# Performance work log

Measured on AMD Instinct MI355X. Metric: run time of the kernel, lower is better.

## Reference

```python
import jax, jax.numpy as jnp
import numpy as np

K = 3        # prediction_steps
SKIP = 1     # skip_step (forward default)
NEG = 64     # opt.negative_samples
EPS = 1e-11  # ExpNLLLoss epsilon


def setup_inputs() -> dict:
    key = jax.random.key(0)
    ks = jax.random.split(key, 8)
    B, C, H, W = 64, 256, 14, 14
    z = jax.random.normal(ks[0], (B, C, H, W), jnp.float32)
    c = jax.random.normal(ks[1], (B, C, H, W), jnp.float32)
    Wk = jax.random.normal(ks[2], (K, C, C), jnp.float32) / np.sqrt(C).astype(np.float32)
    inp = {"z": z, "c": c, "Wk": Wk}
    for k in range(1, K + 1):
        Hp = H - (k + SKIP)
        rows = Hp * W * B
        inp[f"neg_idx_k{k}"] = jax.random.randint(ks[2 + k], (rows * NEG,), 0, rows, dtype=jnp.int32)
    return inp


def _loss_k(z, c, Wk, neg_idx, k):
    # z, c: [B,C,H,W]; Wk: [Co,Ci] (1x1 conv); neg_idx: [(H-k-SKIP)*W*B*NEG]
    B, C, H, W = z.shape
    Hp = H - (k + SKIP)
    zt = z[:, :, k + SKIP:, :]                            # [B,Ci,Hp,W]
    ztwk = jnp.einsum('oc,bchw->hwbo', Wk, zt)            # [Hp,W,B,Co] (1x1 conv + permute(2,3,0,1))
    flat = ztwk.reshape(Hp * W * B, -1)
    shuf = flat[neg_idx].reshape(Hp, W, B, NEG, -1)       # gathered negatives [Hp,W,B,N,Co]
    ctx = jnp.transpose(c[:, :, :Hp, :], (2, 3, 0, 1))    # context c[:,:,:-(k+SKIP),:] -> [Hp,W,B,Co]
    main = jnp.einsum('hwbc,hwbc->hwb', ctx, ztwk)[..., None]   # [Hp,W,B,1]
    negs = jnp.einsum('hwbc,hwbnc->hwbn', ctx, shuf)            # [Hp,W,B,N]
    log_fk = jnp.concatenate([main, negs], axis=-1)             # [Hp,W,B,1+N]
    log_fk = jnp.transpose(log_fk, (2, 3, 0, 1))                # [B,1+N,Hp,W]
    probs = jax.nn.softmax(log_fk, axis=1)
    # ExpNLLLoss, target class 0, reduction='mean'
    return -jnp.mean(jnp.log(probs[:, 0] + EPS))


def reference(z, c, Wk, neg_idx_k1, neg_idx_k2, neg_idx_k3):
    idxs = [neg_idx_k1, neg_idx_k2, neg_idx_k3]
    total = 0.0
    for k in range(1, K + 1):
        total = total + _loss_k(z, c, Wk[k - 1], idxs[k - 1], k)
    return total / K
```

## Files before the change

kernel.cpp:

```cpp
#include <hip/hip_runtime.h>
#include <math.h>


typedef short bf16x8 __attribute__((ext_vector_type(8)));
typedef float f32x4 __attribute__((ext_vector_type(4)));

static __device__ __forceinline__ unsigned short f2bf(float f) {
    union { float f; unsigned int u; } x; x.f = f;
    unsigned int r = x.u + 0x7fffu + ((x.u >> 16) & 1u);
    return (unsigned short)(r >> 16);
}

static __device__ __forceinline__ unsigned char f2e4m3(float f) {
    union { float f; unsigned int u; } x; x.f = f;
    unsigned int s = (x.u >> 24) & 0x80u;
    float af = fabsf(f);
    if (af > 448.f) af = 448.f;
    x.f = af;
    unsigned int u = x.u;
    int e = (int)(u >> 23) - 127;
    unsigned int out;
    if (af == 0.f) {
        out = 0u;
    } else if (e < -6) {
        int mq = (int)rintf(af * 512.f);
        out = (mq >= 8) ? 0x08u : (unsigned int)mq;
    } else {
        unsigned int r = u + 0x7FFFFu + ((u >> 20) & 1u);
        int e2 = (int)(r >> 23) - 127;
        if (e2 > 8) out = 0x7Eu;
        else out = (unsigned int)(((e2 + 7) << 3) | ((r >> 20) & 7u));
    }
    return (unsigned char)(s | out);
}

static __device__ __forceinline__ void gload_lds4(const void* g, void* l) {
    __builtin_amdgcn_global_load_lds(
        (const __attribute__((address_space(1))) void*)g,
        (__attribute__((address_space(3))) void*)l, 4, 0, 0);
}

__global__ __launch_bounds__(256)
void prep_kernel(const float* __restrict__ z, const float* __restrict__ c,
                 const float* __restrict__ Wk,
                 unsigned short* __restrict__ zt, unsigned char* __restrict__ ct8,
                 unsigned short* __restrict__ wkb, float* __restrict__ out) {
    __shared__ float tile[16][201];
    const int tid = threadIdx.x;
    int x = blockIdx.x;
    if (x < 768) {
        int i = x * 256 + tid;
        wkb[i] = f2bf(Wk[i]);
        if (x == 0 && tid == 0) out[0] = 0.f;
        return;
    }
    const bool isz = x < 1792;
    const int local = isz ? (x - 768) : (x - 1792);
    const float* src = isz ? z : c;
    const int b  = local & 63;
    const int c0 = (local >> 6) << 4;
    for (int i = tid; i < 16 * 196; i += 256) {
        int cc = i / 196;
        int hw = i - cc * 196;
        tile[cc][hw] = src[(size_t)((b << 8) + c0 + cc) * 196 + hw];
    }
    __syncthreads();
    if (isz) {
        for (int i = tid; i < 196 * 16; i += 256) {
            int hw = i >> 4, cc = i & 15;
            zt[(size_t)((hw << 6) + b) * 256 + c0 + cc] = f2bf(tile[cc][hw]);
        }
    } else {
        for (int i = tid; i < 196 * 16; i += 256) {
            int hw = i >> 4, cc = i & 15;
            ct8[(size_t)((hw << 6) + b) * 256 + c0 + cc] = f2e4m3(tile[cc][hw]);
        }
    }
}

#define PSTR 528
__global__ __launch_bounds__(256)
void proj_mfma_kernel(const unsigned short* __restrict__ zt,
                      const unsigned short* __restrict__ wkb,
                      unsigned char* __restrict__ ztwk) {
    __shared__ __align__(16) unsigned char smem[(64 + 32) * PSTR];
    unsigned char* smA = smem;
    unsigned char* smB = smem + 64 * PSTR;

    int x = blockIdx.y;
    int k, hw;
    if (x < 168)      { k = 0; hw = x; }
    else if (x < 322) { k = 1; hw = x - 168; }
    else              { k = 2; hw = x - 322; }
    const int o0 = blockIdx.x << 5;
    const int row0  = hw << 6;
    const int zrow0 = row0 + (((k + 2) * 14) << 6);
    unsigned char* zo = ztwk + (size_t)k * 10752 * 256;

    const int tid = threadIdx.x;
    const unsigned char* zsrc = (const unsigned char*)(zt + (size_t)zrow0 * 256);
    const unsigned char* bsrc = (const unsigned char*)(wkb + ((size_t)k << 16) + o0 * 256);

    #pragma unroll
    for (int i = 0; i < 8; ++i) {
        int sb = ((i << 8) + tid) << 4;
        int r = sb >> 9, off = sb & 511;
        *(int4*)(smA + r * PSTR + off) = *(const int4*)(zsrc + sb);
    }
    #pragma unroll
    for (int i = 0; i < 4; ++i) {
        int sb = ((i << 8) + tid) << 4;
        int r = sb >> 9, off = sb & 511;
        *(int4*)(smB + r * PSTR + off) = *(const int4*)(bsrc + sb);
    }
    __syncthreads();

    const int wv = tid >> 6, lane = tid & 63;
    const int m = lane & 15, kq = lane >> 4;
    f32x4 acc[2] = {};
    const unsigned short* aP  = (const unsigned short*)(smA + (size_t)((wv << 4) + m) * PSTR) + (kq << 3);
    const unsigned short* bP0 = (const unsigned short*)(smB + (size_t)m * PSTR) + (kq << 3);
    const unsigned short* bP1 = (const unsigned short*)(smB + (size_t)(16 + m) * PSTR) + (kq << 3);
    #pragma unroll
    for (int kk = 0; kk < 256; kk += 32) {
        bf16x8 af = *(const bf16x8*)(aP  + kk);
        bf16x8 b0 = *(const bf16x8*)(bP0 + kk);
        bf16x8 b1 = *(const bf16x8*)(bP1 + kk);
        acc[0] = __builtin_amdgcn_mfma_f32_16x16x32_bf16(af, b0, acc[0], 0, 0, 0);
        acc[1] = __builtin_amdgcn_mfma_f32_16x16x32_bf16(af, b1, acc[1], 0, 0, 0);
    }
    __syncthreads();
    unsigned char* cs = smA;
    #pragma unroll
    for (int nt = 0; nt < 2; ++nt)
        #pragma unroll
        for (int r = 0; r < 4; ++r)
            cs[(size_t)((wv << 4) + (kq << 2) + r) * 40 + (nt << 4) + m] =
                f2e4m3(acc[nt][r]);
    __syncthreads();
    {
        int r = tid >> 2, off = (tid & 3) << 3;
        unsigned long long v = *(const unsigned long long*)(cs + (size_t)r * 40 + off);
        *(unsigned long long*)(zo + (size_t)(row0 + r) * 256 + o0 + off) = v;
    }
}

#define ROWB 272
__global__ __launch_bounds__(128, 4)
void loss_mfma_kernel(const unsigned char* __restrict__ ct8,
                      const unsigned char* __restrict__ ztwk8,
                      const int* __restrict__ n0, const int* __restrict__ n1,
                      const int* __restrict__ n2, float* __restrict__ rowloss) {
    __shared__ __align__(16) unsigned char slab[65 * ROWB];
    __shared__ __align__(16) unsigned char ctx_s[256];
    __shared__ float sred[2][2];
    const int tid = threadIdx.x;
    const int wv = tid >> 6, lane = tid & 63;
    const int m = lane & 15, kq = lane >> 4;

    int x = blockIdx.x;
    int k; const int* nb_base;
    if (x < 10752)      { k = 0; nb_base = n0; }
    else if (x < 20608) { k = 1; nb_base = n1; x -= 10752; }
    else                { k = 2; nb_base = n2; x -= 20608; }
    const int row = x;
    const unsigned char* flat8 = ztwk8 + (size_t)k * 10752 * 256;
    const float wk = (k == 0) ? (1.f / (3.f * 10752.f))
                   : (k == 1) ? (1.f / (3.f * 9856.f))
                              : (1.f / (3.f * 8960.f));
    const int rbase = (k == 0) ? 0 : (k == 1) ? 10752 : 20608;

    const int myidx = nb_base[((size_t)row << 6) + lane];

    if (wv == 0) {
        gload_lds4(flat8 + (size_t)row * 256 + (lane << 2), slab);
        #pragma unroll
        for (int j = 1; j <= 32; ++j) {
            int idx = __builtin_amdgcn_readlane(myidx, j - 1);
            gload_lds4(flat8 + (size_t)idx * 256 + (lane << 2), slab + j * ROWB);
        }
    } else {
        gload_lds4(ct8 + (size_t)row * 256 + (lane << 2), ctx_s);
        #pragma unroll
        for (int j = 33; j <= 64; ++j) {
            int idx = __builtin_amdgcn_readlane(myidx, j - 1);
            gload_lds4(flat8 + (size_t)idx * 256 + (lane << 2), slab + j * ROWB);
        }
    }
    __syncthreads();

    f32x4 acc[3] = {};
    const int mt0 = (wv == 0) ? 0 : 3;
    int soff[3];
    #pragma unroll
    for (int t = 0; t < 3; ++t) {
        int slot = ((mt0 + t) << 4) + m;
        if (slot > 64) slot = 64;
        soff[t] = slot * ROWB + (kq << 3);
    }
    const unsigned char* cp = ctx_s + (kq << 3);
    #pragma unroll
    for (int kk = 0; kk < 8; ++kk) {
        long long bfrag = *(const long long*)(cp + (kk << 5));
        #pragma unroll
        for (int t = 0; t < 3; ++t) {
            if (t < 2 || wv == 0) {
                long long af = *(const long long*)(slab + soff[t] + (kk << 5));
                acc[t] = __builtin_amdgcn_mfma_f32_16x16x32_fp8_fp8(af, bfrag, acc[t], 0, 0, 0);
            }
        }
    }

    float m_l = -1e30f;
    if (wv == 0) {
        #pragma unroll
        for (int t = 0; t < 3; ++t)
            #pragma unroll
            for (int r = 0; r < 4; ++r) m_l = fmaxf(m_l, acc[t][r]);
    } else {
        #pragma unroll
        for (int r = 0; r < 4; ++r) m_l = fmaxf(m_l, acc[0][r]);
        if (kq == 0) m_l = fmaxf(m_l, acc[1][0]);
    }
    m_l = fmaxf(m_l, __shfl_xor(m_l, 16));
    m_l = fmaxf(m_l, __shfl_xor(m_l, 32));

    float s_l = 0.f;
    if (wv == 0) {
        #pragma unroll
        for (int t = 0; t < 3; ++t)
            #pragma unroll
            for (int r = 0; r < 4; ++r) s_l += __expf(acc[t][r] - m_l);
    } else {
        #pragma unroll
        for (int r = 0; r < 4; ++r) s_l += __expf(acc[0][r] - m_l);
        if (kq == 0) s_l += __expf(acc[1][0] - m_l);
    }
    s_l += __shfl_xor(s_l, 16);
    s_l += __shfl_xor(s_l, 32);

    float main_l = acc[0][0];
    if (lane == 0) { sred[wv][0] = m_l; sred[wv][1] = s_l; }
    __syncthreads();
    if (tid == 0) {
        float m0 = sred[0][0], s0 = sred[0][1];
        float m1 = sred[1][0], s1 = sred[1][1];
        float mg = fmaxf(m0, m1);
        float sg = s0 * __expf(m0 - mg) + s1 * __expf(m1 - mg);
        float p0 = __expf(main_l - mg) / sg;
        rowloss[rbase + row] = -logf(p0 + 1e-11f) * wk;
    }
}

__global__ __launch_bounds__(256)
void reduce_kernel(const float* __restrict__ rl, float* __restrict__ out) {
    float s = 0.f;
    const int stride = gridDim.x * blockDim.x;
    for (int i = blockIdx.x * blockDim.x + threadIdx.x; i < 29568; i += stride)
        s += rl[i];
    #pragma unroll
    for (int off = 32; off >= 1; off >>= 1) s += __shfl_xor(s, off);
    if ((threadIdx.x & 63) == 0) atomicAdd(out, s);
}

extern "C" void kernel_launch(void* const* d_in, const int* in_sizes, int n_in,
                              void* d_out, int out_size, void* d_ws, size_t ws_size,
                              hipStream_t stream) {
    const float* z  = (const float*)d_in[0];
    const float* c  = (const float*)d_in[1];
    const float* Wk = (const float*)d_in[2];
    const int* negs[3] = {(const int*)d_in[3], (const int*)d_in[4], (const int*)d_in[5]};
    float* out = (float*)d_out;

    char* p = (char*)d_ws;
    unsigned short* zt      = (unsigned short*)p;   p += (size_t)196 * 64 * 256 * 2;
    unsigned short* wkb     = (unsigned short*)p;   p += (size_t)3 * 65536 * 2;
    unsigned char*  ct8     = (unsigned char*)p;    p += (size_t)196 * 64 * 256;
    unsigned char*  ztwk8   = (unsigned char*)p;    p += (size_t)3 * 10752 * 256;
    float*          rowloss = (float*)p;

    prep_kernel<<<2816, 256, 0, stream>>>(z, c, Wk, zt, ct8, wkb, out);
    proj_mfma_kernel<<<dim3(8, 462), 256, 0, stream>>>(zt, wkb, ztwk8);
    loss_mfma_kernel<<<29568, 128, 0, stream>>>(ct8, ztwk8, negs[0], negs[1],
                                                negs[2], rowloss);
    reduce_kernel<<<32, 256, 0, stream>>>(rowloss, out);
}
```

Measured before the change: 157.9 us.

## Make loss kernel persistent with double-buffered gather prefetch

The loss kernel changes from one block per row to 1024 persistent blocks that stride over all rows. While the current row is computed, each block gathers the next row's negatives and context into a second LDS buffer, and it preloads the index list two rows ahead. Each block keeps its partial loss in a register and writes one value, so the reduce kernel shrinks to four blocks. This is meant to remove block launch and tail overhead and to hide gather latency, at the cost of twice the LDS per block and fewer resident waves per CU to cover memory latency.

After: 171.0 us. +8.3%, slower.

```diff
diff --git a/kernel.cpp b/kernel.cpp
--- a/kernel.cpp
+++ b/kernel.cpp
@@ -146,118 +146,178 @@
 }
 
 #define ROWB 272
-__global__ __launch_bounds__(128, 4)
+#define NBLK 1024
+
+static __device__ __forceinline__ void rowmeta(int gr, int* k, int* row) {
+    if (gr < 10752)      { *k = 0; *row = gr; }
+    else if (gr < 20608) { *k = 1; *row = gr - 10752; }
+    else                 { *k = 2; *row = gr - 20608; }
+}
+
+__global__ __launch_bounds__(128, 2)
 void loss_mfma_kernel(const unsigned char* __restrict__ ct8,
                       const unsigned char* __restrict__ ztwk8,
                       const int* __restrict__ n0, const int* __restrict__ n1,
                       const int* __restrict__ n2, float* __restrict__ rowloss) {
-    __shared__ __align__(16) unsigned char slab[65 * ROWB];
-    __shared__ __align__(16) unsigned char ctx_s[256];
-    __shared__ float sred[2][2];
+    __shared__ __align__(16) unsigned char slab[2][65 * ROWB];
+    __shared__ __align__(16) unsigned char ctxs[2][256];
+    __shared__ int idxb[2][64];
+    __shared__ float sred[2][2][4];
+
     const int tid = threadIdx.x;
     const int wv = tid >> 6, lane = tid & 63;
     const int m = lane & 15, kq = lane >> 4;
-
-    int x = blockIdx.x;
-    int k; const int* nb_base;
-    if (x < 10752)      { k = 0; nb_base = n0; }
-    else if (x < 20608) { k = 1; nb_base = n1; x -= 10752; }
-    else                { k = 2; nb_base = n2; x -= 20608; }
-    const int row = x;
-    const unsigned char* flat8 = ztwk8 + (size_t)k * 10752 * 256;
-    const float wk = (k == 0) ? (1.f / (3.f * 10752.f))
-                   : (k == 1) ? (1.f / (3.f * 9856.f))
-                              : (1.f / (3.f * 8960.f));
-    const int rbase = (k == 0) ? 0 : (k == 1) ? 10752 : 20608;
-
-    const int myidx = nb_base[((size_t)row << 6) + lane];
-
-    if (wv == 0) {
-        gload_lds4(flat8 + (size_t)row * 256 + (lane << 2), slab);
-        #pragma unroll
-        for (int j = 1; j <= 32; ++j) {
-            int idx = __builtin_amdgcn_readlane(myidx, j - 1);
-            gload_lds4(flat8 + (size_t)idx * 256 + (lane << 2), slab + j * ROWB);
-        }
-    } else {
-        gload_lds4(ct8 + (size_t)row * 256 + (lane << 2), ctx_s);
-        #pragma unroll
-        for (int j = 33; j <= 64; ++j) {
-            int idx = __builtin_amdgcn_readlane(myidx, j - 1);
-            gload_lds4(flat8 + (size_t)idx * 256 + (lane << 2), slab + j * ROWB);
-        }
-    }
-    __syncthreads();
-
-    f32x4 acc[3] = {};
-    const int mt0 = (wv == 0) ? 0 : 3;
-    int soff[3];
-    #pragma unroll
-    for (int t = 0; t < 3; ++t) {
-        int slot = ((mt0 + t) << 4) + m;
-        if (slot > 64) slot = 64;
-        soff[t] = slot * ROWB + (kq << 3);
-    }
-    const unsigned char* cp = ctx_s + (kq << 3);
-    #pragma unroll
-    for (int kk = 0; kk < 8; ++kk) {
-        long long bfrag = *(const long long*)(cp + (kk << 5));
+    const int bid = blockIdx.x;
+    const int n = (29568 - bid + (NBLK - 1)) >> 10;
+
+    float lacc = 0.f;
+
+    if (wv == 0)
+        gload_lds4(n0 + ((size_t)bid << 6) + lane, idxb[0]);
+    __syncthreads();
+    {
+        int myidx = idxb[0][lane];
+        const unsigned char* f8 = ztwk8;
+        if (wv == 0) {
+            gload_lds4(f8 + (size_t)bid * 256 + (lane << 2), slab[0]);
+            #pragma unroll
+            for (int j = 1; j <= 32; ++j) {
+                int idx = __builtin_amdgcn_readlane(myidx, j - 1);
+                gload_lds4(f8 + (size_t)idx * 256 + (lane << 2), slab[0] + j * ROWB);
+            }
+            gload_lds4(n0 + ((size_t)(bid + NBLK) << 6) + lane, idxb[1]);
+        } else {
+            gload_lds4(ct8 + (size_t)bid * 256 + (lane << 2), ctxs[0]);
+            #pragma unroll
+            for (int j = 33; j <= 64; ++j) {
+                int idx = __builtin_amdgcn_readlane(myidx, j - 1);
+                gload_lds4(f8 + (size_t)idx * 256 + (lane << 2), slab[0] + j * ROWB);
+            }
+        }
+    }
+    __syncthreads();
+
+    for (int i = 0; i < n; ++i) {
+        const int p = i & 1;
+        const int gr = bid + (i << 10);
+        int k, row; rowmeta(gr, &k, &row);
+        const float wk = (k == 0) ? (1.f / (3.f * 10752.f))
+                       : (k == 1) ? (1.f / (3.f * 9856.f))
+                                  : (1.f / (3.f * 8960.f));
+
+        const int gr1 = gr + NBLK;
+        if (gr1 < 29568) {
+            int k1, row1; rowmeta(gr1, &k1, &row1);
+            const unsigned char* f81 = ztwk8 + (size_t)k1 * 10752 * 256;
+            int myidx = idxb[p ^ 1][lane];
+            if (wv == 0) {
+                gload_lds4(f81 + (size_t)row1 * 256 + (lane << 2), slab[p ^ 1]);
+                #pragma unroll
+                for (int j = 1; j <= 32; ++j) {
+                    int idx = __builtin_amdgcn_readlane(myidx, j - 1);
+                    gload_lds4(f81 + (size_t)idx * 256 + (lane << 2),
+                               slab[p ^ 1] + j * ROWB);
+                }
+                const int gr2 = gr + 2 * NBLK;
+                if (gr2 < 29568) {
+                    int k2, row2; rowmeta(gr2, &k2, &row2);
+                    const int* nb2 = (k2 == 0) ? n0 : (k2 == 1) ? n1 : n2;
+                    gload_lds4(nb2 + ((size_t)row2 << 6) + lane, idxb[p]);
+                }
+            } else {
+                gload_lds4(ct8 + (size_t)row1 * 256 + (lane << 2), ctxs[p ^ 1]);
+                #pragma unroll
+                for (int j = 33; j <= 64; ++j) {
+                    int idx = __builtin_amdgcn_readlane(myidx, j - 1);
+                    gload_lds4(f81 + (size_t)idx * 256 + (lane << 2),
+                               slab[p ^ 1] + j * ROWB);
+                }
+            }
+        }
+
+        if (i > 0 && tid == 0) {
+            float m0 = sred[p ^ 1][0][0], s0 = sred[p ^ 1][0][1];
+            float m1 = sred[p ^ 1][1][0], s1 = sred[p ^ 1][1][1];
+            float mg = fmaxf(m0, m1);
+            float sg = s0 * __expf(m0 - mg) + s1 * __expf(m1 - mg);
+            float p0 = __expf(sred[p ^ 1][0][2] - mg) / sg;
+            lacc += -logf(p0 + 1e-11f) * sred[p ^ 1][0][3];
+        }
+
+        f32x4 acc[3] = {};
+        const int mt0 = (wv == 0) ? 0 : 3;
+        int soff[3];
         #pragma unroll
         for (int t = 0; t < 3; ++t) {
-            if (t < 2 || wv == 0) {
-                long long af = *(const long long*)(slab + soff[t] + (kk << 5));
-                acc[t] = __builtin_amdgcn_mfma_f32_16x16x32_fp8_fp8(af, bfrag, acc[t], 0, 0, 0);
+            int slot = ((mt0 + t) << 4) + m;
+            if (slot > 64) slot = 64;
+            soff[t] = slot * ROWB + (kq << 3);
+        }
+        const unsigned char* sb = slab[p];
+        const unsigned char* cp = ctxs[p] + (kq << 3);
+        #pragma unroll
+        for (int kk = 0; kk < 8; ++kk) {
+            long long bfrag = *(const long long*)(cp + (kk << 5));
+            #pragma unroll
+            for (int t = 0; t < 3; ++t) {
+                if (t < 2 || wv == 0) {
+                    long long af = *(const long long*)(sb + soff[t] + (kk << 5));
+                    acc[t] = __builtin_amdgcn_mfma_f32_16x16x32_fp8_fp8(af, bfrag, acc[t], 0, 0, 0);
+                }
             }
         }
-    }
-
-    float m_l = -1e30f;
-    if (wv == 0) {
-        #pragma unroll
-        for (int t = 0; t < 3; ++t)
-            #pragma unroll
-            for (int r = 0; r < 4; ++r) m_l = fmaxf(m_l, acc[t][r]);
-    } else {
-        #pragma unroll
-        for (int r = 0; r < 4; ++r) m_l = fmaxf(m_l, acc[0][r]);
-        if (kq == 0) m_l = fmaxf(m_l, acc[1][0]);
-    }
-    m_l = fmaxf(m_l, __shfl_xor(m_l, 16));
-    m_l = fmaxf(m_l, __shfl_xor(m_l, 32));
-
-    float s_l = 0.f;
-    if (wv == 0) {
-        #pragma unroll
-        for (int t = 0; t < 3; ++t)
-            #pragma unroll
-            for (int r = 0; r < 4; ++r) s_l += __expf(acc[t][r] - m_l);
-    } else {
-        #pragma unroll
-        for (int r = 0; r < 4; ++r) s_l += __expf(acc[0][r] - m_l);
-        if (kq == 0) s_l += __expf(acc[1][0] - m_l);
-    }
-    s_l += __shfl_xor(s_l, 16);
-    s_l += __shfl_xor(s_l, 32);
-
-    float main_l = acc[0][0];
-    if (lane == 0) { sred[wv][0] = m_l; sred[wv][1] = s_l; }
-    __syncthreads();
+
+        float m_l = -1e30f;
+        if (wv == 0) {
+            #pragma unroll
+            for (int t = 0; t < 3; ++t)
+                #pragma unroll
+                for (int r = 0; r < 4; ++r) m_l = fmaxf(m_l, acc[t][r]);
+        } else {
+            #pragma unroll
+            for (int r = 0; r < 4; ++r) m_l = fmaxf(m_l, acc[0][r]);
+            if (kq == 0) m_l = fmaxf(m_l, acc[1][0]);
+        }
+        m_l = fmaxf(m_l, __shfl_xor(m_l, 16));
+        m_l = fmaxf(m_l, __shfl_xor(m_l, 32));
+
+        float s_l = 0.f;
+        if (wv == 0) {
+            #pragma unroll
+            for (int t = 0; t < 3; ++t)
+                #pragma unroll
+                for (int r = 0; r < 4; ++r) s_l += __expf(acc[t][r] - m_l);
+        } else {
+            #pragma unroll
+            for (int r = 0; r < 4; ++r) s_l += __expf(acc[0][r] - m_l);
+            if (kq == 0) s_l += __expf(acc[1][0] - m_l);
+        }
+        s_l += __shfl_xor(s_l, 16);
+        s_l += __shfl_xor(s_l, 32);
+
+        if (lane == 0) {
+            sred[p][wv][0] = m_l;
+            sred[p][wv][1] = s_l;
+            if (wv == 0) { sred[p][0][2] = acc[0][0]; sred[p][0][3] = wk; }
+        }
+        __syncthreads();
+    }
+
     if (tid == 0) {
-        float m0 = sred[0][0], s0 = sred[0][1];
-        float m1 = sred[1][0], s1 = sred[1][1];
+        const int q = (n - 1) & 1;
+        float m0 = sred[q][0][0], s0 = sred[q][0][1];
+        float m1 = sred[q][1][0], s1 = sred[q][1][1];
         float mg = fmaxf(m0, m1);
         float sg = s0 * __expf(m0 - mg) + s1 * __expf(m1 - mg);
-        float p0 = __expf(main_l - mg) / sg;
-        rowloss[rbase + row] = -logf(p0 + 1e-11f) * wk;
+        float p0 = __expf(sred[q][0][2] - mg) / sg;
+        lacc += -logf(p0 + 1e-11f) * sred[q][0][3];
+        rowloss[bid] = lacc;
     }
 }
 
 __global__ __launch_bounds__(256)
 void reduce_kernel(const float* __restrict__ rl, float* __restrict__ out) {
-    float s = 0.f;
-    const int stride = gridDim.x * blockDim.x;
-    for (int i = blockIdx.x * blockDim.x + threadIdx.x; i < 29568; i += stride)
-        s += rl[i];
+    float s = rl[blockIdx.x * 256 + threadIdx.x];
     #pragma unroll
     for (int off = 32; off >= 1; off >>= 1) s += __shfl_xor(s, off);
     if ((threadIdx.x & 63) == 0) atomicAdd(out, s);
@@ -281,7 +341,7 @@
 
     prep_kernel<<<2816, 256, 0, stream>>>(z, c, Wk, zt, ct8, wkb, out);
     proj_mfma_kernel<<<dim3(8, 462), 256, 0, stream>>>(zt, wkb, ztwk8);
-    loss_mfma_kernel<<<29568, 128, 0, stream>>>(ct8, ztwk8, negs[0], negs[1],
-                                                negs[2], rowloss);
-    reduce_kernel<<<32, 256, 0, stream>>>(rowloss, out);
-}
+    loss_mfma_kernel<<<NBLK, 128, 0, stream>>>(ct8, ztwk8, negs[0], negs[1],
+                                               negs[2], rowloss);
+    reduce_kernel<<<4, 256, 0, stream>>>(rowloss, out);
+}
```

## Load gathered negatives directly into registers, one wave per row

Applied to the files above, without the earlier changes.

The loss kernel now gives each wave a whole row and drops the LDS slab and block-level sync. Gathered negative rows are loaded straight from global memory into MFMA A fragments with 16-byte vector loads. The loads are software-pipelined two tiles ahead of the MFMA chain. To make those 16-byte loads line up with the fp8 MFMA k-layout, the channel order of ct8 and ztwk8 is permuted in the prep and projection kernels. The cost is much higher register pressure (40 longs of A fragments), which may limit occupancy.

Result: slower. 172.5 us (+9.2%).

```diff
diff --git a/kernel.cpp b/kernel.cpp
--- a/kernel.cpp
+++ b/kernel.cpp
@@ -4,6 +4,7 @@
 
 typedef short bf16x8 __attribute__((ext_vector_type(8)));
 typedef float f32x4 __attribute__((ext_vector_type(4)));
+typedef long long ll2 __attribute__((ext_vector_type(2)));
 
 static __device__ __forceinline__ unsigned short f2bf(float f) {
     union { float f; unsigned int u; } x; x.f = f;
@@ -34,12 +35,6 @@
     return (unsigned char)(s | out);
 }
 
-static __device__ __forceinline__ void gload_lds4(const void* g, void* l) {
-    __builtin_amdgcn_global_load_lds(
-        (const __attribute__((address_space(1))) void*)g,
-        (__attribute__((address_space(3))) void*)l, 4, 0, 0);
-}
-
 __global__ __launch_bounds__(256)
 void prep_kernel(const float* __restrict__ z, const float* __restrict__ c,
                  const float* __restrict__ Wk,
@@ -73,7 +68,10 @@
     } else {
         for (int i = tid; i < 196 * 16; i += 256) {
             int hw = i >> 4, cc = i & 15;
-            ct8[(size_t)((hw << 6) + b) * 256 + c0 + cc] = f2e4m3(tile[cc][hw]);
+            int o = c0 + cc;
+            int n = ((o >> 6) << 6) | (((o >> 3) & 3) << 4)
+                  | (((o >> 5) & 1) << 3) | (o & 7);
+            ct8[(size_t)((hw << 6) + b) * 256 + n] = f2e4m3(tile[cc][hw]);
         }
     }
 }
@@ -141,115 +139,104 @@
     {
         int r = tid >> 2, off = (tid & 3) << 3;
         unsigned long long v = *(const unsigned long long*)(cs + (size_t)r * 40 + off);
-        *(unsigned long long*)(zo + (size_t)(row0 + r) * 256 + o0 + off) = v;
-    }
-}
-
-#define ROWB 272
-__global__ __launch_bounds__(128, 4)
+        *(unsigned long long*)(zo + (size_t)(row0 + r) * 256
+            + ((blockIdx.x >> 1) << 6) + (off << 1) + ((blockIdx.x & 1) << 3)) = v;
+    }
+}
+
+static __device__ __forceinline__ void rowmeta(int gr, int* k, int* row) {
+    if (gr < 10752)      { *k = 0; *row = gr; }
+    else if (gr < 20608) { *k = 1; *row = gr - 10752; }
+    else                 { *k = 2; *row = gr - 20608; }
+}
+
+__global__ __launch_bounds__(256, 4)
 void loss_mfma_kernel(const unsigned char* __restrict__ ct8,
                       const unsigned char* __restrict__ ztwk8,
                       const int* __restrict__ n0, const int* __restrict__ n1,
                       const int* __restrict__ n2, float* __restrict__ rowloss) {
-    __shared__ __align__(16) unsigned char slab[65 * ROWB];
-    __shared__ __align__(16) unsigned char ctx_s[256];
-    __shared__ float sred[2][2];
     const int tid = threadIdx.x;
     const int wv = tid >> 6, lane = tid & 63;
     const int m = lane & 15, kq = lane >> 4;
-
-    int x = blockIdx.x;
-    int k; const int* nb_base;
-    if (x < 10752)      { k = 0; nb_base = n0; }
-    else if (x < 20608) { k = 1; nb_base = n1; x -= 10752; }
-    else                { k = 2; nb_base = n2; x -= 20608; }
-    const int row = x;
-    const unsigned char* flat8 = ztwk8 + (size_t)k * 10752 * 256;
-    const float wk = (k == 0) ? (1.f / (3.f * 10752.f))
-                   : (k == 1) ? (1.f / (3.f * 9856.f))
-                              : (1.f / (3.f * 8960.f));
-    const int rbase = (k == 0) ? 0 : (k == 1) ? 10752 : 20608;
-
-    const int myidx = nb_base[((size_t)row << 6) + lane];
-
-    if (wv == 0) {
-        gload_lds4(flat8 + (size_t)row * 256 + (lane << 2), slab);
-        #pragma unroll
-        for (int j = 1; j <= 32; ++j) {
-            int idx = __builtin_amdgcn_readlane(myidx, j - 1);
-            gload_lds4(flat8 + (size_t)idx * 256 + (lane << 2), slab + j * ROWB);
-        }
-    } else {
-        gload_lds4(ct8 + (size_t)row * 256 + (lane << 2), ctx_s);
-        #pragma unroll
-        for (int j = 33; j <= 64; ++j) {
-            int idx = __builtin_amdgcn_readlane(myidx, j - 1);
-            gload_lds4(flat8 + (size_t)idx * 256 + (lane << 2), slab + j * ROWB);
-        }
-    }
-    __syncthreads();
-
-    f32x4 acc[3] = {};
-    const int mt0 = (wv == 0) ? 0 : 3;
-    int soff[3];
-    #pragma unroll
-    for (int t = 0; t < 3; ++t) {
-        int slot = ((mt0 + t) << 4) + m;
-        if (slot > 64) slot = 64;
-        soff[t] = slot * ROWB + (kq << 3);
-    }
-    const unsigned char* cp = ctx_s + (kq << 3);
-    #pragma unroll
-    for (int kk = 0; kk < 8; ++kk) {
-        long long bfrag = *(const long long*)(cp + (kk << 5));
-        #pragma unroll
-        for (int t = 0; t < 3; ++t) {
-            if (t < 2 || wv == 0) {
-                long long af = *(const long long*)(slab + soff[t] + (kk << 5));
-                acc[t] = __builtin_amdgcn_mfma_f32_16x16x32_fp8_fp8(af, bfrag, acc[t], 0, 0, 0);
+    const int gr = (blockIdx.x << 2) + wv;
+    int k, row; rowmeta(gr, &k, &row);
+    const int* nb = (k == 0) ? n0 : (k == 1) ? n1 : n2;
+    const float wkc = (k == 0) ? (1.f / (3.f * 10752.f))
+                    : (k == 1) ? (1.f / (3.f * 9856.f))
+                               : (1.f / (3.f * 8960.f));
+    const unsigned char* f8 = ztwk8 + (size_t)k * 10752 * 256;
+
+    const int myidx = nb[((size_t)row << 6) + lane];
+
+    long long bf[8];
+    {
+        const unsigned char* cb = ct8 + (size_t)row * 256 + (kq << 4);
+        #pragma unroll
+        for (int c = 0; c < 4; ++c) {
+            ll2 v = *(const ll2*)(cb + (c << 6));
+            bf[2 * c] = v.x; bf[2 * c + 1] = v.y;
+        }
+    }
+
+    int sr[5];
+    #pragma unroll
+    for (int t = 0; t < 5; ++t) {
+        int s = (t << 4) + m; if (s > 64) s = 64;
+        int sel = s - 1; if (sel < 0) sel = 0;
+        int v = __shfl(myidx, sel);
+        sr[t] = (s == 0) ? row : v;
+    }
+
+    long long af[5][8];
+    #pragma unroll
+    for (int t = 0; t < 2; ++t) {
+        const unsigned char* p = f8 + (size_t)sr[t] * 256 + (kq << 4);
+        #pragma unroll
+        for (int c = 0; c < 4; ++c) {
+            ll2 v = *(const ll2*)(p + (c << 6));
+            af[t][2 * c] = v.x; af[t][2 * c + 1] = v.y;
+        }
+    }
+
+    f32x4 acc[5];
+    #pragma unroll
+    for (int t = 0; t < 5; ++t) {
+        if (t + 2 < 5) {
+            const unsigned char* p = f8 + (size_t)sr[t + 2] * 256 + (kq << 4);
+            #pragma unroll
+            for (int c = 0; c < 4; ++c) {
+                ll2 v = *(const ll2*)(p + (c << 6));
+                af[t + 2][2 * c] = v.x; af[t + 2][2 * c + 1] = v.y;
             }
         }
+        f32x4 a = {0.f, 0.f, 0.f, 0.f};
+        #pragma unroll
+        for (int kk = 0; kk < 8; ++kk)
+            a = __builtin_amdgcn_mfma_f32_16x16x32_fp8_fp8(af[t][kk], bf[kk], a, 0, 0, 0);
+        acc[t] = a;
     }
 
     float m_l = -1e30f;
-    if (wv == 0) {
-        #pragma unroll
-        for (int t = 0; t < 3; ++t)
-            #pragma unroll
-            for (int r = 0; r < 4; ++r) m_l = fmaxf(m_l, acc[t][r]);
-    } else {
-        #pragma unroll
-        for (int r = 0; r < 4; ++r) m_l = fmaxf(m_l, acc[0][r]);
-        if (kq == 0) m_l = fmaxf(m_l, acc[1][0]);
-    }
+    #pragma unroll
+    for (int t = 0; t < 4; ++t)
+        #pragma unroll
+        for (int r = 0; r < 4; ++r) m_l = fmaxf(m_l, acc[t][r]);
+    if (kq == 0) m_l = fmaxf(m_l, acc[4][0]);
     m_l = fmaxf(m_l, __shfl_xor(m_l, 16));
     m_l = fmaxf(m_l, __shfl_xor(m_l, 32));
 
     float s_l = 0.f;
-    if (wv == 0) {
-        #pragma unroll
-        for (int t = 0; t < 3; ++t)
-            #pragma unroll
-            for (int r = 0; r < 4; ++r) s_l += __expf(acc[t][r] - m_l);
-    } else {
-        #pragma unroll
-        for (int r = 0; r < 4; ++r) s_l += __expf(acc[0][r] - m_l);
-        if (kq == 0) s_l += __expf(acc[1][0] - m_l);
-    }
+    #pragma unroll
+    for (int t = 0; t < 4; ++t)
+        #pragma unroll
+        for (int r = 0; r < 4; ++r) s_l += __expf(acc[t][r] - m_l);
+    if (kq == 0) s_l += __expf(acc[4][0] - m_l);
     s_l += __shfl_xor(s_l, 16);
     s_l += __shfl_xor(s_l, 32);
 
-    float main_l = acc[0][0];
-    if (lane == 0) { sred[wv][0] = m_l; sred[wv][1] = s_l; }
-    __syncthreads();
-    if (tid == 0) {
-        float m0 = sred[0][0], s0 = sred[0][1];
-        float m1 = sred[1][0], s1 = sred[1][1];
-        float mg = fmaxf(m0, m1);
-        float sg = s0 * __expf(m0 - mg) + s1 * __expf(m1 - mg);
-        float p0 = __expf(main_l - mg) / sg;
-        rowloss[rbase + row] = -logf(p0 + 1e-11f) * wk;
-    }
+    float mainl = __shfl(acc[0][0], 0);
+    if (lane == 0)
+        rowloss[gr] = -logf(__expf(mainl - m_l) / s_l + 1e-11f) * wkc;
 }
 
 __global__ __launch_bounds__(256)
@@ -281,7 +268,7 @@
 
     prep_kernel<<<2816, 256, 0, stream>>>(z, c, Wk, zt, ct8, wkb, out);
     proj_mfma_kernel<<<dim3(8, 462), 256, 0, stream>>>(zt, wkb, ztwk8);
-    loss_mfma_kernel<<<29568, 128, 0, stream>>>(ct8, ztwk8, negs[0], negs[1],
-                                                negs[2], rowloss);
+    loss_mfma_kernel<<<7392, 256, 0, stream>>>(ct8, ztwk8, negs[0], negs[1],
+                                               negs[2], rowloss);
     reduce_kernel<<<32, 256, 0, stream>>>(rowloss, out);
 }
```
